# Kernel tuning notes

Hardware: AMD Instinct MI355X
Metric: run time of the kernel (lower is better)

## Reference

```python
import jax, jax.numpy as jnp
import numpy as np
from jax import lax

NUM_TAGS = 64
PAD = 0


def setup_inputs() -> dict:
    key = jax.random.key(0)
    k1, k2, k3 = jax.random.split(key, 3)
    B, S, T = 128, 512, NUM_TAGS
    features = jax.random.normal(k1, (B, S, T), dtype=jnp.float32)
    labels = jax.random.randint(k2, (B, S), 0, T, dtype=jnp.int64)
    mask = jnp.ones((B, S), dtype=jnp.float32)
    transitions = jax.random.normal(k3, (T, T), dtype=jnp.float32)
    transitions = transitions.at[PAD, :].set(-10000.0)
    transitions = transitions.at[:, PAD].set(-10000.0)
    return {"features": features, "labels": labels, "mask": mask,
            "transitions": transitions}


def _score_sequence(emissions, labels, mask, transitions):
    # emission score at the gold labels, masked
    em = jnp.take_along_axis(emissions, labels[:, :, None], axis=2)[:, :, 0]
    seq_em = jnp.sum(em * mask, axis=1)
    # transition scores between consecutive gold labels
    tr = transitions[labels[:, :-1], labels[:, 1:]]
    tr_mask = mask[:, :-1] * mask[:, 1:]
    seq_tr = jnp.sum(tr * tr_mask, axis=1)
    return seq_em + seq_tr  # (B,)


def _log_partition(emissions, mask, transitions):
    # forward algorithm over the sequence via lax.scan
    alpha0 = emissions[:, 0, :]  # (B, T)
    em_rest = jnp.swapaxes(emissions[:, 1:, :], 0, 1)  # (S-1, B, T)
    mk_rest = jnp.swapaxes(mask[:, 1:], 0, 1)          # (S-1, B)

    def step(alpha, xs):
        em_t, m_t = xs
        # scores[b, i, j] = alpha[b, i] + transitions[i, j] + em_t[b, j]
        scores = alpha[:, :, None] + transitions[None, :, :] + em_t[:, None, :]
        new_alpha = jax.nn.logsumexp(scores, axis=1)  # (B, T)
        m = m_t[:, None]
        new_alpha = new_alpha * m + alpha * (1.0 - m)
        return new_alpha, None

    alpha, _ = lax.scan(step, alpha0, (em_rest, mk_rest))
    return jax.nn.logsumexp(alpha, axis=1)  # (B,)


def reference(features, labels, mask, transitions):
    gold = _score_sequence(features, labels, mask, transitions)
    logZ = _log_partition(features, mask, transitions)
    return jnp.mean(logZ - gold)  # scalar NLL
```

## Files before the change

kernel.cpp:

```cpp
#include <hip/hip_runtime.h>

#define B 128
#define S 512
#define T 64
#define G 16
#define CL 32

typedef short bf16x8 __attribute__((ext_vector_type(8)));
typedef float f32x4 __attribute__((ext_vector_type(4)));
typedef _Float16 h2 __attribute__((ext_vector_type(2)));
typedef _Float16 h8 __attribute__((ext_vector_type(8)));

__device__ __forceinline__ float rdlane(float v, int l) {
    return __int_as_float(__builtin_amdgcn_readlane(__float_as_int(v), l));
}
__device__ __forceinline__ unsigned cvtpk_bf16(float lo, float hi) {
    unsigned r;
    asm("v_cvt_pk_bf16_f32 %0, %1, %2" : "=v"(r) : "v"(lo), "v"(hi));
    return r;
}
__device__ __forceinline__ unsigned cvt_pkrtz_u(float lo, float hi) {
    unsigned r;
    asm("v_cvt_pkrtz_f16_f32 %0, %1, %2" : "=v"(r) : "v"(lo), "v"(hi));
    return r;
}
__device__ __forceinline__ float fast_exp2(float x) {
    float r;
    asm("v_exp_f32 %0, %1" : "=v"(r) : "v"(x));
    return r;
}
__device__ __forceinline__ int krow(int kt, int gq, int e) {
    return 32 * kt + ((e >> 2) << 4) + 4 * gq + (e & 3);
}

__global__ __launch_bounds__(64, 1)
void crf_chunk(const float* __restrict__ features,
               const float* __restrict__ mask,
               const float* __restrict__ transitions,
               unsigned short* __restrict__ Zout,
               int* __restrict__ Kout)
{
    __shared__ unsigned short relay[T * 68];

    const int lane = threadIdx.x;
    const int b  = blockIdx.x >> 4;
    const int g  = blockIdx.x & (G - 1);
    const int c  = lane & 15;
    const int gq = lane >> 4;

    h8 Ef[4][2];
    float emaxv = 1e-10f;
    #pragma unroll
    for (int rt = 0; rt < 4; ++rt)
      #pragma unroll
      for (int kt = 0; kt < 2; ++kt)
        #pragma unroll
        for (int e = 0; e < 8; ++e) {
            int k = krow(kt, gq, e);
            float x = __expf(transitions[k * T + (c + 16*rt)]);
            emaxv = fmaxf(emaxv, x);
            Ef[rt][kt][e] = (_Float16)x;
        }
    #pragma unroll
    for (int o = 32; o > 0; o >>= 1)
        emaxv = fmaxf(emaxv, __shfl_xor(emaxv, o));
    const float dmax = 60000.0f / emaxv;

    h8 Bf[2][4];
    #pragma unroll
    for (int kt = 0; kt < 2; ++kt)
      #pragma unroll
      for (int ct = 0; ct < 4; ++ct)
        #pragma unroll
        for (int e = 0; e < 8; ++e)
            Bf[kt][ct][e] = (krow(kt, gq, e) == 16*ct + c) ? (_Float16)1.0f
                                                           : (_Float16)0.0f;

    const float* fb   = features + (size_t)b * S * T;
    const float* colp = fb + c;
    const int t0 = g * CL + 1;
    const int t1 = (g == G - 1) ? S : (t0 + CL);

    int kcur = 0, ktot = 0;

    float emN[4];
    #pragma unroll
    for (int rt = 0; rt < 4; ++rt) emN[rt] = colp[t0 * T + 16*rt];
    float mA = mask[(size_t)b * S + t0];

    for (int t = t0; t < t1; ++t) {
        float emc[4];
        #pragma unroll
        for (int rt = 0; rt < 4; ++rt) emc[rt] = emN[rt];
        float m = mA;
        if (t + 1 < t1) {
            #pragma unroll
            for (int rt = 0; rt < 4; ++rt)
                emN[rt] = colp[(t + 1) * T + 16*rt];
            mA = mask[(size_t)b * S + t + 1];
        }
        if (m != 0.0f) {
            const float kcf = (float)kcur;
            h8 Ap[4][2];
            #pragma unroll
            for (int rt = 0; rt < 4; ++rt) {
                float d = fast_exp2(fmaf(emc[rt], 1.44269504f, -kcf));
                d = fminf(d, dmax);
                unsigned w = cvt_pkrtz_u(d, d);
                uint4 qs; qs.x = w; qs.y = w; qs.z = w; qs.w = w;
                h8 ds = __builtin_bit_cast(h8, qs);
                Ap[rt][0] = Ef[rt][0] * ds;
                Ap[rt][1] = Ef[rt][1] * ds;
            }

            f32x4 C[4][4];
            #pragma unroll
            for (int tr = 0; tr < 4; ++tr)
              #pragma unroll
              for (int ct = 0; ct < 4; ++ct) {
                  f32x4 z = {0.f, 0.f, 0.f, 0.f};
                  z = __builtin_amdgcn_mfma_f32_16x16x32_f16(Ap[tr][0], Bf[0][ct], z, 0, 0, 0);
                  z = __builtin_amdgcn_mfma_f32_16x16x32_f16(Ap[tr][1], Bf[1][ct], z, 0, 0, 0);
                  C[tr][ct] = z;
              }

            float mx = 1e-30f;
            #pragma unroll
            for (int tr = 0; tr < 4; ++tr)
              #pragma unroll
              for (int ct = 0; ct < 4; ++ct) {
                  float m01 = fmaxf(C[tr][ct][0], C[tr][ct][1]);
                  float m23 = fmaxf(C[tr][ct][2], C[tr][ct][3]);
                  mx = fmaxf(mx, fmaxf(m01, m23));
              }
            #pragma unroll
            for (int o = 32; o > 0; o >>= 1)
                mx = fmaxf(mx, __shfl_xor(mx, o));
            ktot += kcur;
            kcur = (((__float_as_int(mx) >> 23) & 0xFF) - 127) + 8;
            kcur = kcur < -60 ? -60 : (kcur > 60 ? 60 : kcur);

            #pragma unroll
            for (int kt = 0; kt < 2; ++kt)
              #pragma unroll
              for (int ct = 0; ct < 4; ++ct) {
                  uint4 q;
                  q.x = cvt_pkrtz_u(C[2*kt  ][ct][0], C[2*kt  ][ct][1]);
                  q.y = cvt_pkrtz_u(C[2*kt  ][ct][2], C[2*kt  ][ct][3]);
                  q.z = cvt_pkrtz_u(C[2*kt+1][ct][0], C[2*kt+1][ct][1]);
                  q.w = cvt_pkrtz_u(C[2*kt+1][ct][2], C[2*kt+1][ct][3]);
                  Bf[kt][ct] = __builtin_bit_cast(h8, q);
              }
        }
    }

    #pragma unroll
    for (int kt = 0; kt < 2; ++kt)
      #pragma unroll
      for (int ct = 0; ct < 4; ++ct) {
          int col = 16*ct + c;
          unsigned dw[4];
          #pragma unroll
          for (int p = 0; p < 4; ++p)
              dw[p] = cvtpk_bf16((float)Bf[kt][ct][2*p], (float)Bf[kt][ct][2*p+1]);
          uint2 wa; wa.x = dw[0]; wa.y = dw[1];
          uint2 wb; wb.x = dw[2]; wb.y = dw[3];
          *(uint2*)&relay[col * 68 + 32*kt      + 4*gq] = wa;
          *(uint2*)&relay[col * 68 + 32*kt + 16 + 4*gq] = wb;
      }
    asm volatile("s_waitcnt lgkmcnt(0)" ::: "memory");

    unsigned short* zo = Zout + ((size_t)(b * G + g)) * 64 * 64;
    #pragma unroll
    for (int q8 = 0; q8 < 8; ++q8) {
        unsigned dw[4];
        #pragma unroll
        for (int d = 0; d < 4; ++d) {
            unsigned lo = relay[(8*q8 + 2*d    ) * 68 + lane];
            unsigned hi = relay[(8*q8 + 2*d + 1) * 68 + lane];
            dw[d] = lo | (hi << 16);
        }
        uint4 w; w.x = dw[0]; w.y = dw[1]; w.z = dw[2]; w.w = dw[3];
        *(uint4*)(zo + (size_t)lane * 64 + 8*q8) = w;
    }
    if (lane == 0) Kout[b * G + g] = ktot;
}

__global__ __launch_bounds__(64, 1)
void crf_apply(const float* __restrict__ features,
               const int*   __restrict__ labels,
               const float* __restrict__ mask,
               const float* __restrict__ transitions,
               const unsigned short* __restrict__ Zmat,
               const int*   __restrict__ Kscale,
               float*       __restrict__ res)
{
    __shared__ float trans_lds[T * T];
    __shared__ float bcast[2][T];
    const int lane = threadIdx.x;
    const int b = blockIdx.x;

    for (int i = 0; i < T; ++i)
        trans_lds[i * T + lane] = transitions[i * T + lane];
    __syncthreads();

    const float* fb = features + (size_t)b * S * T;
    const int*   lb = labels + (size_t)b * S;
    const float* mb = mask + (size_t)b * S;

    float gold = 0.f;
    #pragma unroll
    for (int ch = 0; ch < S / T; ++ch) {
        int tt = ch * T + lane;
        int tm1 = tt > 0 ? tt - 1 : 0;
        int la = lb[tt], lp = lb[tm1];
        float mt = mb[tt], mp = mb[tm1];
        float em_g = fb[(size_t)tt * T + la];
        float tr_g = trans_lds[lp * T + la];
        gold += em_g * mt + ((tt > 0) ? tr_g * (mp * mt) : 0.f);
    }

    float a0 = fb[lane];
    float A0 = a0;
    #pragma unroll
    for (int o = 32; o > 0; o >>= 1) A0 = fmaxf(A0, __shfl_xor(A0, o));
    float v = __expf(a0 - A0);
    float off = A0;

    const unsigned short* zb = Zmat + ((size_t)b * G) * 64 * 64 + (size_t)lane * 64;
    uint4 cur[8], nxt[8];
    #pragma unroll
    for (int i = 0; i < 8; ++i) cur[i] = ((const uint4*)zb)[i];

    for (int g = 0; g < G; ++g) {
        if (g + 1 < G) {
            const uint4* zn = (const uint4*)(zb + (size_t)(g + 1) * 64 * 64);
            #pragma unroll
            for (int i = 0; i < 8; ++i) nxt[i] = zn[i];
        }
        const int buf = g & 1;
        bcast[buf][lane] = v;
        asm volatile("s_waitcnt lgkmcnt(0)" ::: "memory");
        f32x4 vb[16];
        #pragma unroll
        for (int q = 0; q < 16; ++q) vb[q] = ((const f32x4*)bcast[buf])[q];

        float acc = 0.f;
        #pragma unroll
        for (int i = 0; i < 8; ++i) {
            unsigned zz[4] = {cur[i].x, cur[i].y, cur[i].z, cur[i].w};
            #pragma unroll
            for (int d = 0; d < 4; ++d) {
                int k = i * 8 + d * 2;
                float f0 = __int_as_float(zz[d] << 16);
                float f1 = __int_as_float(zz[d] & 0xFFFF0000u);
                acc = fmaf(f0, vb[k >> 2][k & 3], acc);
                acc = fmaf(f1, vb[(k + 1) >> 2][(k + 1) & 3], acc);
            }
        }
        acc = fminf(fmaxf(acc, 0.f), 1e30f);
        float r = acc;
        #pragma unroll
        for (int o = 32; o > 0; o >>= 1) r = fmaxf(r, __shfl_xor(r, o));
        r = fmaxf(r, 1e-30f);
        v = acc / r;
        off += __logf(r) + (float)Kscale[b * G + g] * 0.69314718056f;
        #pragma unroll
        for (int i = 0; i < 8; ++i) cur[i] = nxt[i];
    }

    float sum = v;
    #pragma unroll
    for (int o = 32; o > 0; o >>= 1) sum += __shfl_xor(sum, o);
    float logZ = __logf(fmaxf(sum, 1e-30f)) + off;

    #pragma unroll
    for (int o = 32; o > 0; o >>= 1) gold += __shfl_xor(gold, o);

    if (lane == 0) res[b] = logZ - gold;
}

__global__ __launch_bounds__(64, 1)
void crf_fwd_seq(const float* __restrict__ features,
                 const int*   __restrict__ labels,
                 const float* __restrict__ mask,
                 const float* __restrict__ transitions,
                 float*       __restrict__ ws)
{
    __shared__ float trans_lds[T * T];
    __shared__ __align__(16) _Float16 ea_lds[2][T];

    const int lane = threadIdx.x;
    const int b    = blockIdx.x;

    for (int i = 0; i < T; ++i)
        trans_lds[i * T + lane] = transitions[i * T + lane];
    __syncthreads();

    h2 etr[T / 2];
    #pragma unroll
    for (int k = 0; k < T / 2; ++k) {
        etr[k].x = (_Float16)__expf(trans_lds[(2 * k + 0) * T + lane]);
        etr[k].y = (_Float16)__expf(trans_lds[(2 * k + 1) * T + lane]);
    }

    const float* fb = features + (size_t)b * S * T;
    const float* mb = mask + (size_t)b * S;
    const int*   lb = labels + (size_t)b * S;

    float alpha = fb[lane];
    float gold_part = 0.f;
    float M = 0.f;

    float em_n1 = fb[1 * T + lane];
    float em_n2 = fb[2 * T + lane];
    float em_n3 = fb[3 * T + lane];

    int   lab_c = lb[lane];
    int   lab_p = lb[lane > 0 ? lane - 1 : 0];
    float m_c   = mb[lane];
    float m_p   = mb[lane > 0 ? lane - 1 : 0];

    for (int ch = 0; ch < S / T; ++ch) {
        const int base = ch * T;
        const int tt   = base + lane;

        const int   glab  = lab_c;
        const int   glabp = lab_p;
        const float gmc   = m_c;
        const float gmp   = m_p;
        const float mreg  = m_c;

        float em_g = fb[(size_t)tt * T + glab];
        float tr_g = trans_lds[glabp * T + glab];

        {
            int tn  = tt + T;  if (tn > S - 1) tn = S - 1;
            int tnp = tn - 1;  if (tnp < 0) tnp = 0;
            lab_c = lb[tn]; lab_p = lb[tnp];
            m_c   = mb[tn]; m_p   = mb[tnp];
        }

        const int i0 = (ch == 0) ? 1 : 0;
        #pragma unroll 4
        for (int i = i0; i < T; ++i) {
            const int t = base + i;
            float em = em_n1;
            em_n1 = em_n2; em_n2 = em_n3;
            int tn = t + 3; if (tn > S - 1) tn = S - 1;
            em_n3 = fb[tn * T + lane];

            float ea = __expf(alpha - M);
            ea_lds[t & 1][lane] = (_Float16)ea;
            asm volatile("s_waitcnt lgkmcnt(0)" ::: "memory");

            const uint4* ep = (const uint4*)&ea_lds[t & 1][0];
            float a0 = 0.f, a1 = 0.f, a2 = 0.f, a3 = 0.f;
            #pragma unroll
            for (int q = 0; q < 8; ++q) {
                uint4 r = ep[q];
                a0 = __builtin_amdgcn_fdot2(__builtin_bit_cast(h2, r.x), etr[4 * q + 0], a0, false);
                a1 = __builtin_amdgcn_fdot2(__builtin_bit_cast(h2, r.y), etr[4 * q + 1], a1, false);
                a2 = __builtin_amdgcn_fdot2(__builtin_bit_cast(h2, r.z), etr[4 * q + 2], a2, false);
                a3 = __builtin_amdgcn_fdot2(__builtin_bit_cast(h2, r.w), etr[4 * q + 3], a3, false);
            }
            float s = (a0 + a1) + (a2 + a3);

            float m_t = rdlane(mreg, i);
            float s1  = rdlane(s, 1);
            float em1 = rdlane(em, 1);
            float Mn  = M + __logf(s1) + em1;

            float val = M + __logf(s) + em;
            val = fmaxf(val, -1e30f);
            alpha = val * m_t + alpha * (1.f - m_t);
            M     = (m_t > 0.5f) ? Mn : M;
        }

        float valid = (tt > 0) ? 1.f : 0.f;
        gold_part += em_g * gmc + tr_g * (gmp * gmc) * valid;
    }

    float M2 = alpha;
    #pragma unroll
    for (int o = 32; o > 0; o >>= 1) M2 = fmaxf(M2, __shfl_xor(M2, o));
    float e2 = __expf(alpha - M2);
    #pragma unroll
    for (int o = 32; o > 0; o >>= 1) e2 += __shfl_xor(e2, o);
    float logZ = M2 + __logf(e2);

    #pragma unroll
    for (int o = 32; o > 0; o >>= 1) gold_part += __shfl_xor(gold_part, o);

    if (lane == 0) ws[b] = logZ - gold_part;
}

__global__ __launch_bounds__(128)
void crf_reduce(const float* __restrict__ ws, float* __restrict__ out)
{
    const int tid = threadIdx.x;
    float v = ws[tid];
    #pragma unroll
    for (int o = 32; o > 0; o >>= 1) v += __shfl_xor(v, o);

    __shared__ float partial[2];
    if ((tid & 63) == 0) partial[tid >> 6] = v;
    __syncthreads();
    if (tid == 0) out[0] = (partial[0] + partial[1]) * (1.0f / (float)B);
}

extern "C" void kernel_launch(void* const* d_in, const int* in_sizes, int n_in,
                              void* d_out, int out_size, void* d_ws, size_t ws_size,
                              hipStream_t stream)
{
    const float* features    = (const float*)d_in[0];
    const int*   labels      = (const int*)  d_in[1];
    const float* mask        = (const float*)d_in[2];
    const float* transitions = (const float*)d_in[3];
    float* out = (float*)d_out;

    const size_t zbytes = (size_t)B * G * 64 * 64 * sizeof(unsigned short);
    const size_t kbytes = (size_t)B * G * sizeof(int);
    const size_t need   = zbytes + kbytes + (size_t)B * sizeof(float);

    if (ws_size >= need) {
        unsigned short* Zmat = (unsigned short*)d_ws;
        int*   Ks  = (int*)((char*)d_ws + zbytes);
        float* res = (float*)((char*)d_ws + zbytes + kbytes);
        crf_chunk<<<dim3(B * G), dim3(64), 0, stream>>>(features, mask, transitions, Zmat, Ks);
        crf_apply<<<dim3(B), dim3(64), 0, stream>>>(features, labels, mask, transitions, Zmat, Ks, res);
        crf_reduce<<<dim3(1), dim3(128), 0, stream>>>(res, out);
    } else {
        float* res = (float*)d_ws;
        crf_fwd_seq<<<dim3(B), dim3(64), 0, stream>>>(features, labels, mask, transitions, res);
        crf_reduce<<<dim3(1), dim3(128), 0, stream>>>(res, out);
    }
}
```

Baseline: 68.20 us.

## Split sequence into 32 chunks, raise chunk occupancy, interleave MFMA column tiles

Templates the chunk and apply kernels on the chunk count and launches 32 chunks per sequence when the workspace allows, halving the serial length of each chunk's transfer-matrix product. Launch bounds on the chunk kernel now allow 3 waves per SIMD. The MFMA loop is restructured per column tile so results are converted and max-reduced immediately, which lowers live registers. In exchange the apply kernel walks twice as many 64x64 matrices serially and twice the intermediate data is written and read.

```diff
diff --git a/kernel.cpp b/kernel.cpp
--- a/kernel.cpp
+++ b/kernel.cpp
@@ -3,10 +3,7 @@
 #define B 128
 #define S 512
 #define T 64
-#define G 16
-#define CL 32
-
-typedef short bf16x8 __attribute__((ext_vector_type(8)));
+
 typedef float f32x4 __attribute__((ext_vector_type(4)));
 typedef _Float16 h2 __attribute__((ext_vector_type(2)));
 typedef _Float16 h8 __attribute__((ext_vector_type(8)));
@@ -33,18 +30,20 @@
     return 32 * kt + ((e >> 2) << 4) + 4 * gq + (e & 3);
 }
 
-__global__ __launch_bounds__(64, 1)
+template<int GG>
+__global__ __launch_bounds__(64, 3)
 void crf_chunk(const float* __restrict__ features,
                const float* __restrict__ mask,
                const float* __restrict__ transitions,
                unsigned short* __restrict__ Zout,
                int* __restrict__ Kout)
 {
+    constexpr int CLT = S / GG;
     __shared__ unsigned short relay[T * 68];
 
     const int lane = threadIdx.x;
-    const int b  = blockIdx.x >> 4;
-    const int g  = blockIdx.x & (G - 1);
+    const int b  = blockIdx.x / GG;
+    const int g  = blockIdx.x % GG;
     const int c  = lane & 15;
     const int gq = lane >> 4;
 
@@ -78,8 +77,8 @@
 
     const float* fb   = features + (size_t)b * S * T;
     const float* colp = fb + c;
-    const int t0 = g * CL + 1;
-    const int t1 = (g == G - 1) ? S : (t0 + CL);
+    const int t0 = g * CLT + 1;
+    const int t1 = (g == GG - 1) ? S : (t0 + CLT);
 
     int kcur = 0, ktot = 0;
 
@@ -113,44 +112,40 @@
                 Ap[rt][1] = Ef[rt][1] * ds;
             }
 
-            f32x4 C[4][4];
-            #pragma unroll
-            for (int tr = 0; tr < 4; ++tr)
-              #pragma unroll
-              for (int ct = 0; ct < 4; ++ct) {
-                  f32x4 z = {0.f, 0.f, 0.f, 0.f};
-                  z = __builtin_amdgcn_mfma_f32_16x16x32_f16(Ap[tr][0], Bf[0][ct], z, 0, 0, 0);
-                  z = __builtin_amdgcn_mfma_f32_16x16x32_f16(Ap[tr][1], Bf[1][ct], z, 0, 0, 0);
-                  C[tr][ct] = z;
-              }
-
             float mx = 1e-30f;
             #pragma unroll
-            for (int tr = 0; tr < 4; ++tr)
-              #pragma unroll
-              for (int ct = 0; ct < 4; ++ct) {
-                  float m01 = fmaxf(C[tr][ct][0], C[tr][ct][1]);
-                  float m23 = fmaxf(C[tr][ct][2], C[tr][ct][3]);
-                  mx = fmaxf(mx, fmaxf(m01, m23));
-              }
+            for (int ct = 0; ct < 4; ++ct) {
+                f32x4 Ct[4];
+                #pragma unroll
+                for (int tr = 0; tr < 4; ++tr) {
+                    f32x4 z = {0.f, 0.f, 0.f, 0.f};
+                    z = __builtin_amdgcn_mfma_f32_16x16x32_f16(Ap[tr][0], Bf[0][ct], z, 0, 0, 0);
+                    z = __builtin_amdgcn_mfma_f32_16x16x32_f16(Ap[tr][1], Bf[1][ct], z, 0, 0, 0);
+                    Ct[tr] = z;
+                }
+                #pragma unroll
+                for (int tr = 0; tr < 4; ++tr)
+                    mx = fmaxf(mx, fmaxf(fmaxf(Ct[tr][0], Ct[tr][1]),
+                                         fmaxf(Ct[tr][2], Ct[tr][3])));
+                uint4 q0, q1;
+                q0.x = cvt_pkrtz_u(Ct[0][0], Ct[0][1]);
+                q0.y = cvt_pkrtz_u(Ct[0][2], Ct[0][3]);
+                q0.z = cvt_pkrtz_u(Ct[1][0], Ct[1][1]);
+                q0.w = cvt_pkrtz_u(Ct[1][2], Ct[1][3]);
+                q1.x = cvt_pkrtz_u(Ct[2][0], Ct[2][1]);
+                q1.y = cvt_pkrtz_u(Ct[2][2], Ct[2][3]);
+                q1.z = cvt_pkrtz_u(Ct[3][0], Ct[3][1]);
+                q1.w = cvt_pkrtz_u(Ct[3][2], Ct[3][3]);
+                Bf[0][ct] = __builtin_bit_cast(h8, q0);
+                Bf[1][ct] = __builtin_bit_cast(h8, q1);
+            }
+
             #pragma unroll
             for (int o = 32; o > 0; o >>= 1)
                 mx = fmaxf(mx, __shfl_xor(mx, o));
             ktot += kcur;
             kcur = (((__float_as_int(mx) >> 23) & 0xFF) - 127) + 8;
             kcur = kcur < -60 ? -60 : (kcur > 60 ? 60 : kcur);
-
-            #pragma unroll
-            for (int kt = 0; kt < 2; ++kt)
-              #pragma unroll
-              for (int ct = 0; ct < 4; ++ct) {
-                  uint4 q;
-                  q.x = cvt_pkrtz_u(C[2*kt  ][ct][0], C[2*kt  ][ct][1]);
-                  q.y = cvt_pkrtz_u(C[2*kt  ][ct][2], C[2*kt  ][ct][3]);
-                  q.z = cvt_pkrtz_u(C[2*kt+1][ct][0], C[2*kt+1][ct][1]);
-                  q.w = cvt_pkrtz_u(C[2*kt+1][ct][2], C[2*kt+1][ct][3]);
-                  Bf[kt][ct] = __builtin_bit_cast(h8, q);
-              }
         }
     }
 
@@ -170,7 +165,7 @@
       }
     asm volatile("s_waitcnt lgkmcnt(0)" ::: "memory");
 
-    unsigned short* zo = Zout + ((size_t)(b * G + g)) * 64 * 64;
+    unsigned short* zo = Zout + ((size_t)(b * GG + g)) * 64 * 64;
     #pragma unroll
     for (int q8 = 0; q8 < 8; ++q8) {
         unsigned dw[4];
@@ -183,9 +178,10 @@
         uint4 w; w.x = dw[0]; w.y = dw[1]; w.z = dw[2]; w.w = dw[3];
         *(uint4*)(zo + (size_t)lane * 64 + 8*q8) = w;
     }
-    if (lane == 0) Kout[b * G + g] = ktot;
-}
-
+    if (lane == 0) Kout[b * GG + g] = ktot;
+}
+
+template<int GG>
 __global__ __launch_bounds__(64, 1)
 void crf_apply(const float* __restrict__ features,
                const int*   __restrict__ labels,
@@ -227,13 +223,13 @@
     float v = __expf(a0 - A0);
     float off = A0;
 
-    const unsigned short* zb = Zmat + ((size_t)b * G) * 64 * 64 + (size_t)lane * 64;
+    const unsigned short* zb = Zmat + ((size_t)b * GG) * 64 * 64 + (size_t)lane * 64;
     uint4 cur[8], nxt[8];
     #pragma unroll
     for (int i = 0; i < 8; ++i) cur[i] = ((const uint4*)zb)[i];
 
-    for (int g = 0; g < G; ++g) {
-        if (g + 1 < G) {
+    for (int g = 0; g < GG; ++g) {
+        if (g + 1 < GG) {
             const uint4* zn = (const uint4*)(zb + (size_t)(g + 1) * 64 * 64);
             #pragma unroll
             for (int i = 0; i < 8; ++i) nxt[i] = zn[i];
@@ -264,7 +260,7 @@
         for (int o = 32; o > 0; o >>= 1) r = fmaxf(r, __shfl_xor(r, o));
         r = fmaxf(r, 1e-30f);
         v = acc / r;
-        off += __logf(r) + (float)Kscale[b * G + g] * 0.69314718056f;
+        off += __logf(r) + (float)Kscale[b * GG + g] * 0.69314718056f;
         #pragma unroll
         for (int i = 0; i < 8; ++i) cur[i] = nxt[i];
     }
@@ -419,16 +415,30 @@
     const float* transitions = (const float*)d_in[3];
     float* out = (float*)d_out;
 
-    const size_t zbytes = (size_t)B * G * 64 * 64 * sizeof(unsigned short);
-    const size_t kbytes = (size_t)B * G * sizeof(int);
-    const size_t need   = zbytes + kbytes + (size_t)B * sizeof(float);
-
-    if (ws_size >= need) {
+    auto need = [](int GG) {
+        return (size_t)B * GG * 64 * 64 * sizeof(unsigned short)
+             + (size_t)B * GG * sizeof(int) + (size_t)B * sizeof(float);
+    };
+
+    if (ws_size >= need(32)) {
+        constexpr int GG = 32;
+        size_t zbytes = (size_t)B * GG * 64 * 64 * sizeof(unsigned short);
+        size_t kbytes = (size_t)B * GG * sizeof(int);
         unsigned short* Zmat = (unsigned short*)d_ws;
         int*   Ks  = (int*)((char*)d_ws + zbytes);
         float* res = (float*)((char*)d_ws + zbytes + kbytes);
-        crf_chunk<<<dim3(B * G), dim3(64), 0, stream>>>(features, mask, transitions, Zmat, Ks);
-        crf_apply<<<dim3(B), dim3(64), 0, stream>>>(features, labels, mask, transitions, Zmat, Ks, res);
+        crf_chunk<GG><<<dim3(B * GG), dim3(64), 0, stream>>>(features, mask, transitions, Zmat, Ks);
+        crf_apply<GG><<<dim3(B), dim3(64), 0, stream>>>(features, labels, mask, transitions, Zmat, Ks, res);
+        crf_reduce<<<dim3(1), dim3(128), 0, stream>>>(res, out);
+    } else if (ws_size >= need(16)) {
+        constexpr int GG = 16;
+        size_t zbytes = (size_t)B * GG * 64 * 64 * sizeof(unsigned short);
+        size_t kbytes = (size_t)B * GG * sizeof(int);
+        unsigned short* Zmat = (unsigned short*)d_ws;
+        int*   Ks  = (int*)((char*)d_ws + zbytes);
+        float* res = (float*)((char*)d_ws + zbytes + kbytes);
+        crf_chunk<GG><<<dim3(B * GG), dim3(64), 0, stream>>>(features, mask, transitions, Zmat, Ks);
+        crf_apply<GG><<<dim3(B), dim3(64), 0, stream>>>(features, labels, mask, transitions, Zmat, Ks, res);
         crf_reduce<<<dim3(1), dim3(128), 0, stream>>>(res, out);
     } else {
         float* res = (float*)d_ws;
```

Measured after the change: 76.16 us. 11.7% more time.

## Interleave two independent chunk chains per wave to hide MFMA latency

Applied to the files above, without the earlier changes.

The chunk kernel now has each 64-thread block advance two independent sequence chunks in lockstep, so the MFMA and reduction dependency chains of one chunk can overlap with the other's. It also deepens the emission prefetch to two steps ahead and fuses the max and the f16 repack into the per-column MFMA loop. The apply kernel splits its dot product into four accumulators to shorten the serial FMA chain. In exchange the grid is halved to 1024 blocks and register pressure roughly doubles, which could reduce occupancy or cause spills.

```diff
diff --git a/kernel.cpp b/kernel.cpp
--- a/kernel.cpp
+++ b/kernel.cpp
@@ -4,9 +4,7 @@
 #define S 512
 #define T 64
 #define G 16
-#define CL 32
-
-typedef short bf16x8 __attribute__((ext_vector_type(8)));
+
 typedef float f32x4 __attribute__((ext_vector_type(4)));
 typedef _Float16 h2 __attribute__((ext_vector_type(2)));
 typedef _Float16 h8 __attribute__((ext_vector_type(8)));
@@ -33,18 +31,22 @@
     return 32 * kt + ((e >> 2) << 4) + 4 * gq + (e & 3);
 }
 
-__global__ __launch_bounds__(64, 1)
-void crf_chunk(const float* __restrict__ features,
-               const float* __restrict__ mask,
-               const float* __restrict__ transitions,
-               unsigned short* __restrict__ Zout,
-               int* __restrict__ Kout)
+template<int GG>
+__global__ __launch_bounds__(64, 2)
+void crf_chunk2(const float* __restrict__ features,
+                const float* __restrict__ mask,
+                const float* __restrict__ transitions,
+                unsigned short* __restrict__ Zout,
+                int* __restrict__ Kout)
 {
+    constexpr int CLT = S / GG;
     __shared__ unsigned short relay[T * 68];
 
     const int lane = threadIdx.x;
-    const int b  = blockIdx.x >> 4;
-    const int g  = blockIdx.x & (G - 1);
+    const int idx  = blockIdx.x;
+    const int b  = idx / (GG / 2);
+    const int q  = idx % (GG / 2);
+    const int g0 = 2 * q, g1 = 2 * q + 1;
     const int c  = lane & 15;
     const int gq = lane >> 4;
 
@@ -66,45 +68,65 @@
         emaxv = fmaxf(emaxv, __shfl_xor(emaxv, o));
     const float dmax = 60000.0f / emaxv;
 
-    h8 Bf[2][4];
+    h8 BfA[2][4], BfB[2][4];
     #pragma unroll
     for (int kt = 0; kt < 2; ++kt)
       #pragma unroll
       for (int ct = 0; ct < 4; ++ct)
         #pragma unroll
-        for (int e = 0; e < 8; ++e)
-            Bf[kt][ct][e] = (krow(kt, gq, e) == 16*ct + c) ? (_Float16)1.0f
-                                                           : (_Float16)0.0f;
+        for (int e = 0; e < 8; ++e) {
+            _Float16 idv = (krow(kt, gq, e) == 16*ct + c) ? (_Float16)1.0f
+                                                          : (_Float16)0.0f;
+            BfA[kt][ct][e] = idv;
+            BfB[kt][ct][e] = idv;
+        }
 
     const float* fb   = features + (size_t)b * S * T;
     const float* colp = fb + c;
-    const int t0 = g * CL + 1;
-    const int t1 = (g == G - 1) ? S : (t0 + CL);
-
-    int kcur = 0, ktot = 0;
-
-    float emN[4];
-    #pragma unroll
-    for (int rt = 0; rt < 4; ++rt) emN[rt] = colp[t0 * T + 16*rt];
-    float mA = mask[(size_t)b * S + t0];
-
-    for (int t = t0; t < t1; ++t) {
-        float emc[4];
-        #pragma unroll
-        for (int rt = 0; rt < 4; ++rt) emc[rt] = emN[rt];
-        float m = mA;
-        if (t + 1 < t1) {
-            #pragma unroll
-            for (int rt = 0; rt < 4; ++rt)
-                emN[rt] = colp[(t + 1) * T + 16*rt];
-            mA = mask[(size_t)b * S + t + 1];
-        }
-        if (m != 0.0f) {
-            const float kcf = (float)kcur;
+    const float* mb   = mask + (size_t)b * S;
+    const int t0A = g0 * CLT + 1;
+    const int t0B = g1 * CLT + 1;
+    const int t1B = (g1 == GG - 1) ? S : (t0B + CLT);
+
+    int kcurA = 0, ktotA = 0, kcurB = 0, ktotB = 0;
+
+    float emA1[4], emA2[4], emB1[4], emB2[4];
+    #pragma unroll
+    for (int rt = 0; rt < 4; ++rt) {
+        emA1[rt] = colp[(t0A    ) * T + 16*rt];
+        emA2[rt] = colp[(t0A + 1) * T + 16*rt];
+        emB1[rt] = colp[(t0B    ) * T + 16*rt];
+        emB2[rt] = colp[(t0B + 1) * T + 16*rt];
+    }
+    float mA1 = mb[t0A], mA2 = mb[t0A + 1];
+    float mB1 = mb[t0B], mB2 = mb[min(t0B + 1, S - 1)];
+
+    for (int i = 0; i < CLT; ++i) {
+        const int tA = t0A + i;
+        const int tB = t0B + i;
+        const bool actB = (tB < t1B);
+
+        float emcA[4], emcB[4];
+        #pragma unroll
+        for (int rt = 0; rt < 4; ++rt) { emcA[rt] = emA1[rt]; emcB[rt] = emB1[rt]; }
+        float mcA = mA1, mcB = mB1;
+        {
+            int tA2 = min(tA + 2, S - 1), tB2 = min(tB + 2, S - 1);
+            #pragma unroll
+            for (int rt = 0; rt < 4; ++rt) {
+                emA1[rt] = emA2[rt];  emA2[rt] = colp[tA2 * T + 16*rt];
+                emB1[rt] = emB2[rt];  emB2[rt] = colp[tB2 * T + 16*rt];
+            }
+            mA1 = mA2; mA2 = mb[tA2];
+            mB1 = mB2; mB2 = mb[tB2];
+        }
+
+        if (mcA != 0.0f) {
+            const float kcf = (float)kcurA;
             h8 Ap[4][2];
             #pragma unroll
             for (int rt = 0; rt < 4; ++rt) {
-                float d = fast_exp2(fmaf(emc[rt], 1.44269504f, -kcf));
+                float d = fast_exp2(fmaf(emcA[rt], 1.44269504f, -kcf));
                 d = fminf(d, dmax);
                 unsigned w = cvt_pkrtz_u(d, d);
                 uint4 qs; qs.x = w; qs.y = w; qs.z = w; qs.w = w;
@@ -112,80 +134,129 @@
                 Ap[rt][0] = Ef[rt][0] * ds;
                 Ap[rt][1] = Ef[rt][1] * ds;
             }
-
-            f32x4 C[4][4];
-            #pragma unroll
-            for (int tr = 0; tr < 4; ++tr)
-              #pragma unroll
-              for (int ct = 0; ct < 4; ++ct) {
-                  f32x4 z = {0.f, 0.f, 0.f, 0.f};
-                  z = __builtin_amdgcn_mfma_f32_16x16x32_f16(Ap[tr][0], Bf[0][ct], z, 0, 0, 0);
-                  z = __builtin_amdgcn_mfma_f32_16x16x32_f16(Ap[tr][1], Bf[1][ct], z, 0, 0, 0);
-                  C[tr][ct] = z;
-              }
-
             float mx = 1e-30f;
             #pragma unroll
-            for (int tr = 0; tr < 4; ++tr)
-              #pragma unroll
-              for (int ct = 0; ct < 4; ++ct) {
-                  float m01 = fmaxf(C[tr][ct][0], C[tr][ct][1]);
-                  float m23 = fmaxf(C[tr][ct][2], C[tr][ct][3]);
-                  mx = fmaxf(mx, fmaxf(m01, m23));
-              }
+            for (int ct = 0; ct < 4; ++ct) {
+                f32x4 Ct[4];
+                #pragma unroll
+                for (int tr = 0; tr < 4; ++tr) {
+                    f32x4 z = {0.f, 0.f, 0.f, 0.f};
+                    z = __builtin_amdgcn_mfma_f32_16x16x32_f16(Ap[tr][0], BfA[0][ct], z, 0, 0, 0);
+                    z = __builtin_amdgcn_mfma_f32_16x16x32_f16(Ap[tr][1], BfA[1][ct], z, 0, 0, 0);
+                    Ct[tr] = z;
+                }
+                #pragma unroll
+                for (int tr = 0; tr < 4; ++tr)
+                    mx = fmaxf(mx, fmaxf(fmaxf(Ct[tr][0], Ct[tr][1]),
+                                         fmaxf(Ct[tr][2], Ct[tr][3])));
+                uint4 q0v, q1v;
+                q0v.x = cvt_pkrtz_u(Ct[0][0], Ct[0][1]);
+                q0v.y = cvt_pkrtz_u(Ct[0][2], Ct[0][3]);
+                q0v.z = cvt_pkrtz_u(Ct[1][0], Ct[1][1]);
+                q0v.w = cvt_pkrtz_u(Ct[1][2], Ct[1][3]);
+                q1v.x = cvt_pkrtz_u(Ct[2][0], Ct[2][1]);
+                q1v.y = cvt_pkrtz_u(Ct[2][2], Ct[2][3]);
+                q1v.z = cvt_pkrtz_u(Ct[3][0], Ct[3][1]);
+                q1v.w = cvt_pkrtz_u(Ct[3][2], Ct[3][3]);
+                BfA[0][ct] = __builtin_bit_cast(h8, q0v);
+                BfA[1][ct] = __builtin_bit_cast(h8, q1v);
+            }
             #pragma unroll
             for (int o = 32; o > 0; o >>= 1)
                 mx = fmaxf(mx, __shfl_xor(mx, o));
-            ktot += kcur;
-            kcur = (((__float_as_int(mx) >> 23) & 0xFF) - 127) + 8;
-            kcur = kcur < -60 ? -60 : (kcur > 60 ? 60 : kcur);
-
-            #pragma unroll
-            for (int kt = 0; kt < 2; ++kt)
+            ktotA += kcurA;
+            kcurA = (((__float_as_int(mx) >> 23) & 0xFF) - 127) + 8;
+            kcurA = kcurA < -60 ? -60 : (kcurA > 60 ? 60 : kcurA);
+        }
+
+        if (actB && mcB != 0.0f) {
+            const float kcf = (float)kcurB;
+            h8 Ap[4][2];
+            #pragma unroll
+            for (int rt = 0; rt < 4; ++rt) {
+                float d = fast_exp2(fmaf(emcB[rt], 1.44269504f, -kcf));
+                d = fminf(d, dmax);
+                unsigned w = cvt_pkrtz_u(d, d);
+                uint4 qs; qs.x = w; qs.y = w; qs.z = w; qs.w = w;
+                h8 ds = __builtin_bit_cast(h8, qs);
+                Ap[rt][0] = Ef[rt][0] * ds;
+                Ap[rt][1] = Ef[rt][1] * ds;
+            }
+            float mx = 1e-30f;
+            #pragma unroll
+            for (int ct = 0; ct < 4; ++ct) {
+                f32x4 Ct[4];
+                #pragma unroll
+                for (int tr = 0; tr < 4; ++tr) {
+                    f32x4 z = {0.f, 0.f, 0.f, 0.f};
+                    z = __builtin_amdgcn_mfma_f32_16x16x32_f16(Ap[tr][0], BfB[0][ct], z, 0, 0, 0);
+                    z = __builtin_amdgcn_mfma_f32_16x16x32_f16(Ap[tr][1], BfB[1][ct], z, 0, 0, 0);
+                    Ct[tr] = z;
+                }
+                #pragma unroll
+                for (int tr = 0; tr < 4; ++tr)
+                    mx = fmaxf(mx, fmaxf(fmaxf(Ct[tr][0], Ct[tr][1]),
+                                         fmaxf(Ct[tr][2], Ct[tr][3])));
+                uint4 q0v, q1v;
+                q0v.x = cvt_pkrtz_u(Ct[0][0], Ct[0][1]);
+                q0v.y = cvt_pkrtz_u(Ct[0][2], Ct[0][3]);
+                q0v.z = cvt_pkrtz_u(Ct[1][0], Ct[1][1]);
+                q0v.w = cvt_pkrtz_u(Ct[1][2], Ct[1][3]);
+                q1v.x = cvt_pkrtz_u(Ct[2][0], Ct[2][1]);
+                q1v.y = cvt_pkrtz_u(Ct[2][2], Ct[2][3]);
+                q1v.z = cvt_pkrtz_u(Ct[3][0], Ct[3][1]);
+                q1v.w = cvt_pkrtz_u(Ct[3][2], Ct[3][3]);
+                BfB[0][ct] = __builtin_bit_cast(h8, q0v);
+                BfB[1][ct] = __builtin_bit_cast(h8, q1v);
+            }
+            #pragma unroll
+            for (int o = 32; o > 0; o >>= 1)
+                mx = fmaxf(mx, __shfl_xor(mx, o));
+            ktotB += kcurB;
+            kcurB = (((__float_as_int(mx) >> 23) & 0xFF) - 127) + 8;
+            kcurB = kcurB < -60 ? -60 : (kcurB > 60 ? 60 : kcurB);
+        }
+    }
+
+    #pragma unroll
+    for (int chain = 0; chain < 2; ++chain) {
+        h8 (*Bf)[4] = chain ? BfB : BfA;
+        const int g = chain ? g1 : g0;
+        #pragma unroll
+        for (int kt = 0; kt < 2; ++kt)
+          #pragma unroll
+          for (int ct = 0; ct < 4; ++ct) {
+              int col = 16*ct + c;
+              unsigned dw[4];
               #pragma unroll
-              for (int ct = 0; ct < 4; ++ct) {
-                  uint4 q;
-                  q.x = cvt_pkrtz_u(C[2*kt  ][ct][0], C[2*kt  ][ct][1]);
-                  q.y = cvt_pkrtz_u(C[2*kt  ][ct][2], C[2*kt  ][ct][3]);
-                  q.z = cvt_pkrtz_u(C[2*kt+1][ct][0], C[2*kt+1][ct][1]);
-                  q.w = cvt_pkrtz_u(C[2*kt+1][ct][2], C[2*kt+1][ct][3]);
-                  Bf[kt][ct] = __builtin_bit_cast(h8, q);
-              }
-        }
-    }
-
-    #pragma unroll
-    for (int kt = 0; kt < 2; ++kt)
-      #pragma unroll
-      for (int ct = 0; ct < 4; ++ct) {
-          int col = 16*ct + c;
-          unsigned dw[4];
-          #pragma unroll
-          for (int p = 0; p < 4; ++p)
-              dw[p] = cvtpk_bf16((float)Bf[kt][ct][2*p], (float)Bf[kt][ct][2*p+1]);
-          uint2 wa; wa.x = dw[0]; wa.y = dw[1];
-          uint2 wb; wb.x = dw[2]; wb.y = dw[3];
-          *(uint2*)&relay[col * 68 + 32*kt      + 4*gq] = wa;
-          *(uint2*)&relay[col * 68 + 32*kt + 16 + 4*gq] = wb;
-      }
-    asm volatile("s_waitcnt lgkmcnt(0)" ::: "memory");
-
-    unsigned short* zo = Zout + ((size_t)(b * G + g)) * 64 * 64;
-    #pragma unroll
-    for (int q8 = 0; q8 < 8; ++q8) {
-        unsigned dw[4];
-        #pragma unroll
-        for (int d = 0; d < 4; ++d) {
-            unsigned lo = relay[(8*q8 + 2*d    ) * 68 + lane];
-            unsigned hi = relay[(8*q8 + 2*d + 1) * 68 + lane];
-            dw[d] = lo | (hi << 16);
-        }
-        uint4 w; w.x = dw[0]; w.y = dw[1]; w.z = dw[2]; w.w = dw[3];
-        *(uint4*)(zo + (size_t)lane * 64 + 8*q8) = w;
-    }
-    if (lane == 0) Kout[b * G + g] = ktot;
-}
-
+              for (int p = 0; p < 4; ++p)
+                  dw[p] = cvtpk_bf16((float)Bf[kt][ct][2*p], (float)Bf[kt][ct][2*p+1]);
+              uint2 wa; wa.x = dw[0]; wa.y = dw[1];
+              uint2 wb; wb.x = dw[2]; wb.y = dw[3];
+              *(uint2*)&relay[col * 68 + 32*kt      + 4*gq] = wa;
+              *(uint2*)&relay[col * 68 + 32*kt + 16 + 4*gq] = wb;
+          }
+        asm volatile("s_waitcnt lgkmcnt(0)" ::: "memory");
+
+        unsigned short* zo = Zout + ((size_t)(b * GG + g)) * 64 * 64;
+        #pragma unroll
+        for (int q8 = 0; q8 < 8; ++q8) {
+            unsigned dw[4];
+            #pragma unroll
+            for (int d = 0; d < 4; ++d) {
+                unsigned lo = relay[(8*q8 + 2*d    ) * 68 + lane];
+                unsigned hi = relay[(8*q8 + 2*d + 1) * 68 + lane];
+                dw[d] = lo | (hi << 16);
+            }
+            uint4 w; w.x = dw[0]; w.y = dw[1]; w.z = dw[2]; w.w = dw[3];
+            *(uint4*)(zo + (size_t)lane * 64 + 8*q8) = w;
+        }
+        asm volatile("s_waitcnt lgkmcnt(0)" ::: "memory");
+        if (lane == 0) Kout[b * GG + g] = chain ? ktotB : ktotA;
+    }
+}
+
+template<int GG>
 __global__ __launch_bounds__(64, 1)
 void crf_apply(const float* __restrict__ features,
                const int*   __restrict__ labels,
@@ -227,13 +298,13 @@
     float v = __expf(a0 - A0);
     float off = A0;
 
-    const unsigned short* zb = Zmat + ((size_t)b * G) * 64 * 64 + (size_t)lane * 64;
+    const unsigned short* zb = Zmat + ((size_t)b * GG) * 64 * 64 + (size_t)lane * 64;
     uint4 cur[8], nxt[8];
     #pragma unroll
     for (int i = 0; i < 8; ++i) cur[i] = ((const uint4*)zb)[i];
 
-    for (int g = 0; g < G; ++g) {
-        if (g + 1 < G) {
+    for (int g = 0; g < GG; ++g) {
+        if (g + 1 < GG) {
             const uint4* zn = (const uint4*)(zb + (size_t)(g + 1) * 64 * 64);
             #pragma unroll
             for (int i = 0; i < 8; ++i) nxt[i] = zn[i];
@@ -245,7 +316,7 @@
         #pragma unroll
         for (int q = 0; q < 16; ++q) vb[q] = ((const f32x4*)bcast[buf])[q];
 
-        float acc = 0.f;
+        float ac0 = 0.f, ac1 = 0.f, ac2 = 0.f, ac3 = 0.f;
         #pragma unroll
         for (int i = 0; i < 8; ++i) {
             unsigned zz[4] = {cur[i].x, cur[i].y, cur[i].z, cur[i].w};
@@ -254,17 +325,20 @@
                 int k = i * 8 + d * 2;
                 float f0 = __int_as_float(zz[d] << 16);
                 float f1 = __int_as_float(zz[d] & 0xFFFF0000u);
-                acc = fmaf(f0, vb[k >> 2][k & 3], acc);
-                acc = fmaf(f1, vb[(k + 1) >> 2][(k + 1) & 3], acc);
-            }
-        }
+                if ((d & 1) == 0) { ac0 = fmaf(f0, vb[k >> 2][k & 3], ac0);
+                                    ac1 = fmaf(f1, vb[(k+1) >> 2][(k+1) & 3], ac1); }
+                else             { ac2 = fmaf(f0, vb[k >> 2][k & 3], ac2);
+                                    ac3 = fmaf(f1, vb[(k+1) >> 2][(k+1) & 3], ac3); }
+            }
+        }
+        float acc = (ac0 + ac1) + (ac2 + ac3);
         acc = fminf(fmaxf(acc, 0.f), 1e30f);
         float r = acc;
         #pragma unroll
         for (int o = 32; o > 0; o >>= 1) r = fmaxf(r, __shfl_xor(r, o));
         r = fmaxf(r, 1e-30f);
         v = acc / r;
-        off += __logf(r) + (float)Kscale[b * G + g] * 0.69314718056f;
+        off += __logf(r) + (float)Kscale[b * GG + g] * 0.69314718056f;
         #pragma unroll
         for (int i = 0; i < 8; ++i) cur[i] = nxt[i];
     }
@@ -427,8 +501,8 @@
         unsigned short* Zmat = (unsigned short*)d_ws;
         int*   Ks  = (int*)((char*)d_ws + zbytes);
         float* res = (float*)((char*)d_ws + zbytes + kbytes);
-        crf_chunk<<<dim3(B * G), dim3(64), 0, stream>>>(features, mask, transitions, Zmat, Ks);
-        crf_apply<<<dim3(B), dim3(64), 0, stream>>>(features, labels, mask, transitions, Zmat, Ks, res);
+        crf_chunk2<G><<<dim3(B * G / 2), dim3(64), 0, stream>>>(features, mask, transitions, Zmat, Ks);
+        crf_apply<G><<<dim3(B), dim3(64), 0, stream>>>(features, labels, mask, transitions, Zmat, Ks, res);
         crf_reduce<<<dim3(1), dim3(128), 0, stream>>>(res, out);
     } else {
         float* res = (float*)d_ws;
```

New measurement: 78.16 us. +14.6%, slower.
